# Performance work log

Hardware: AMD Instinct MI355X
Metric: run time of the kernel (lower is better)

The kernel has to match this reference:

```python
import jax, jax.numpy as jnp
import numpy as np
import math

B, M, C = 256, 256, 1024
ALPHA = 0.1

def setup_inputs() -> dict:
    key = jax.random.key(0)
    k1, k2 = jax.random.split(key)
    input_encoded = jax.random.normal(k1, (B, C), dtype=jnp.float32)
    memory_mean = jax.random.normal(k2, (M, C), dtype=jnp.float32)
    return {"input_encoded": input_encoded, "memory_mean": memory_mean}

def reference(input_encoded, memory_mean):
    b, c = input_encoded.shape
    m = memory_mean.shape[0]
    # ---- write_to_memory ----
    # similarity of each input with each prior memory slot: [B, M]
    sims = jnp.einsum('bc,mc->bm', input_encoded, memory_mean)
    closest_idx = jnp.argmax(sims, axis=1)                      # [B]
    sel = memory_mean[closest_idx]                              # [B, C]
    new_row = (1.0 - ALPHA) * sel + ALPHA * input_encoded       # [B, C]
    onehot = (jnp.arange(m)[None, :] == closest_idx[:, None])   # [B, M] bool
    mem = jnp.broadcast_to(memory_mean[None], (b, m, c))
    updated_memory = jnp.where(onehot[:, :, None], new_row[:, None, :], mem)  # [B, M, C]
    dkl_write = 0.5 * jnp.sum((input_encoded - sel) ** 2, axis=1)             # [B]
    # ---- read_with_encoded_input ----
    scale = 1.0 / math.sqrt(c)
    scores = jnp.einsum('bc,bmc->bm', input_encoded, updated_memory) * scale  # [B, M]
    attn = jax.nn.softmax(scores, axis=1)
    z_read = jnp.einsum('bm,bmc->bc', attn, updated_memory)                   # [B, C]
    dkl_read = 0.5 * jnp.sum((z_read - input_encoded) ** 2, axis=1)           # [B]
    kl_div = dkl_write + dkl_read
    return z_read, updated_memory, kl_div
```

## Files before the change

### kernel.cpp

```cpp
#include <hip/hip_runtime.h>
#include <math.h>

#define B_DIM 256
#define M_DIM 256
#define C_DIM 1024
#define C4 256
#define Z_OFF   0
#define UM_OFF  (B_DIM * C_DIM)
#define KL_OFF  (UM_OFF + B_DIM * M_DIM * C_DIM)
#define SCALE   0.03125f

typedef float nfloat4 __attribute__((ext_vector_type(4)));

__device__ __forceinline__ float block_sum8(float v, float* s_w, int lane, int wv) {
    #pragma unroll
    for (int off = 32; off; off >>= 1) v += __shfl_xor(v, off, 64);
    if (lane == 0) s_w[wv] = v;
    __syncthreads();
    float r = s_w[0] + s_w[1] + s_w[2] + s_w[3]
            + s_w[4] + s_w[5] + s_w[6] + s_w[7];
    __syncthreads();
    return r;
}

__device__ __forceinline__ float block_max8(float v, float* s_w, int lane, int wv) {
    #pragma unroll
    for (int off = 32; off; off >>= 1) v = fmaxf(v, __shfl_xor(v, off, 64));
    if (lane == 0) s_w[wv] = v;
    __syncthreads();
    float r = fmaxf(fmaxf(fmaxf(s_w[0], s_w[1]), fmaxf(s_w[2], s_w[3])),
                    fmaxf(fmaxf(s_w[4], s_w[5]), fmaxf(s_w[6], s_w[7])));
    __syncthreads();
    return r;
}

__global__ __launch_bounds__(512) void tm_fused(const float* __restrict__ x,
                                                const float* __restrict__ mem,
                                                float* __restrict__ out) {
    const int b = blockIdx.x;
    const int t = threadIdx.x;
    const int lane = t & 63;
    const int wv = t >> 6;

    __shared__ float4 s_x4[C4];
    __shared__ float  s_sims[M_DIM];
    __shared__ float  s_attn[M_DIM];
    __shared__ float4 s_z4[C4];
    __shared__ float  s_w[8];
    __shared__ float  s_av[4];
    __shared__ int    s_ai[4];
    __shared__ int    s_idx;
    __shared__ float  s_vidx;

    const float4* mem4 = (const float4*)mem;
    const float4* x4row = (const float4*)(x + (size_t)b * C_DIM);

    float4 xt = make_float4(0.f, 0.f, 0.f, 0.f);
    float p = 0.f;
    if (t < C4) {
        xt = x4row[t];
        s_x4[t] = xt;
        p = xt.x * xt.x + xt.y * xt.y + xt.z * xt.z + xt.w * xt.w;
    }
    const float n2 = block_sum8(p, s_w, lane, wv);

    float4 xr0 = s_x4[lane];
    float4 xr1 = s_x4[lane + 64];
    float4 xr2 = s_x4[lane + 128];
    float4 xr3 = s_x4[lane + 192];
    for (int i = 0; i < 32; ++i) {
        const int m = (i << 3) | wv;
        const float4* mr = mem4 + (size_t)m * C4;
        float4 a0 = mr[lane];
        float4 a1 = mr[lane + 64];
        float4 a2 = mr[lane + 128];
        float4 a3 = mr[lane + 192];
        float acc = a0.x * xr0.x + a0.y * xr0.y + a0.z * xr0.z + a0.w * xr0.w
                  + a1.x * xr1.x + a1.y * xr1.y + a1.z * xr1.z + a1.w * xr1.w
                  + a2.x * xr2.x + a2.y * xr2.y + a2.z * xr2.z + a2.w * xr2.w
                  + a3.x * xr3.x + a3.y * xr3.y + a3.z * xr3.z + a3.w * xr3.w;
        #pragma unroll
        for (int off = 32; off; off >>= 1) acc += __shfl_xor(acc, off, 64);
        if (lane == 0) s_sims[m] = acc;
    }
    __syncthreads();

    float av = -INFINITY;
    int   ai = 0x7fffffff;
    if (t < M_DIM) { av = s_sims[t]; ai = t; }
    #pragma unroll
    for (int off = 32; off; off >>= 1) {
        float ov = __shfl_xor(av, off, 64);
        int   oi = __shfl_xor(ai, off, 64);
        if (ov > av || (ov == av && oi < ai)) { av = ov; ai = oi; }
    }
    if (lane == 0 && wv < 4) { s_av[wv] = av; s_ai[wv] = ai; }
    __syncthreads();
    if (t == 0) {
        float bv = s_av[0]; int bi = s_ai[0];
        #pragma unroll
        for (int w = 1; w < 4; ++w) {
            float v2 = s_av[w]; int i2 = s_ai[w];
            if (v2 > bv || (v2 == bv && i2 < bi)) { bv = v2; bi = i2; }
        }
        s_idx = bi; s_vidx = bv;
    }
    __syncthreads();
    const int idx = s_idx;
    const float sim_idx = s_vidx;

    float sc = -INFINITY;
    if (t < M_DIM)
        sc = (t == idx) ? (0.9f * sim_idx + 0.1f * n2) * SCALE
                        : s_sims[t] * SCALE;
    const float mx = block_max8(sc, s_w, lane, wv);
    float e = (t < M_DIM) ? expf(sc - mx) : 0.f;
    const float esum = block_sum8(e, s_w, lane, wv);
    if (t < M_DIM) s_attn[t] = e / esum;

    float dwp = 0.f;
    if (t < C4) {
        float4 sl = mem4[(size_t)idx * C4 + t];
        float d0 = xt.x - sl.x, d1 = xt.y - sl.y, d2 = xt.z - sl.z, d3 = xt.w - sl.w;
        dwp = d0 * d0 + d1 * d1 + d2 * d2 + d3 * d3;
    }
    const float dw = block_sum8(dwp, s_w, lane, wv);

    const int tc = t & 255;
    const int mbase = (t >> 8) << 7;
    const float4 xc = s_x4[tc];
    float4 z = make_float4(0.f, 0.f, 0.f, 0.f);
    nfloat4* um4 = (nfloat4*)((float4*)(out + UM_OFF) + (size_t)b * M_DIM * C4 + tc);
    for (int i = 0; i < 128; ++i) {
        const int m = mbase + i;
        float4 v = mem4[(size_t)m * C4 + tc];
        if (m == idx) {
            v.x = 0.9f * v.x + 0.1f * xc.x;
            v.y = 0.9f * v.y + 0.1f * xc.y;
            v.z = 0.9f * v.z + 0.1f * xc.z;
            v.w = 0.9f * v.w + 0.1f * xc.w;
        }
        const float a = s_attn[m];
        z.x = fmaf(a, v.x, z.x);
        z.y = fmaf(a, v.y, z.y);
        z.z = fmaf(a, v.z, z.z);
        z.w = fmaf(a, v.w, z.w);
        nfloat4 nv = { v.x, v.y, v.z, v.w };
        __builtin_nontemporal_store(nv, um4 + (size_t)m * C4);
    }

    if (t >= 256) s_z4[tc] = z;
    __syncthreads();
    float drp = 0.f;
    if (t < 256) {
        float4 zo = s_z4[tc];
        z.x += zo.x; z.y += zo.y; z.z += zo.z; z.w += zo.w;
        float d0 = z.x - xc.x, d1 = z.y - xc.y, d2 = z.z - xc.z, d3 = z.w - xc.w;
        drp = d0 * d0 + d1 * d1 + d2 * d2 + d3 * d3;
        ((float4*)(out + Z_OFF))[(size_t)b * C4 + t] = z;
    }
    const float dr = block_sum8(drp, s_w, lane, wv);

    if (t == 0) out[KL_OFF + b] = 0.5f * (dw + dr);
}

extern "C" void kernel_launch(void* const* d_in, const int* in_sizes, int n_in,
                              void* d_out, int out_size, void* d_ws, size_t ws_size,
                              hipStream_t stream) {
    const float* x   = (const float*)d_in[0];
    const float* mem = (const float*)d_in[1];
    float* out = (float*)d_out;

    tm_fused<<<dim3(B_DIM), dim3(512), 0, stream>>>(x, mem, out);
}
```

Before: 70.95 us.

## Use 1024-thread blocks, split memory rows four ways, fold selected-row update algebraically

Doubles the threads per block so each block handles its batch row with 16 waves. Each quarter of the threads now covers 64 memory rows instead of 128, and the partial z sums are combined through shared memory. The attention accumulation now uses the original memory row, and the alpha update of the selected row is added once at the end as attn[idx]*0.1*(x - sel). This takes the conditional out of the dependency chain, and the loop is unrolled by 4. The aim is more memory-level parallelism on the large updated-memory write stream, at the cost of wider block-level reductions and more shared memory.

```diff
diff --git a/kernel.cpp b/kernel.cpp
--- a/kernel.cpp
+++ b/kernel.cpp
@@ -12,64 +12,66 @@
 
 typedef float nfloat4 __attribute__((ext_vector_type(4)));
 
-__device__ __forceinline__ float block_sum8(float v, float* s_w, int lane, int wv) {
+__device__ __forceinline__ float block_sum16(float v, float* s_w, int lane, int wv) {
     #pragma unroll
     for (int off = 32; off; off >>= 1) v += __shfl_xor(v, off, 64);
     if (lane == 0) s_w[wv] = v;
     __syncthreads();
-    float r = s_w[0] + s_w[1] + s_w[2] + s_w[3]
-            + s_w[4] + s_w[5] + s_w[6] + s_w[7];
+    float r = 0.f;
+    #pragma unroll
+    for (int w = 0; w < 16; ++w) r += s_w[w];
     __syncthreads();
     return r;
 }
 
-__device__ __forceinline__ float block_max8(float v, float* s_w, int lane, int wv) {
+__device__ __forceinline__ float block_max16(float v, float* s_w, int lane, int wv) {
     #pragma unroll
     for (int off = 32; off; off >>= 1) v = fmaxf(v, __shfl_xor(v, off, 64));
     if (lane == 0) s_w[wv] = v;
     __syncthreads();
-    float r = fmaxf(fmaxf(fmaxf(s_w[0], s_w[1]), fmaxf(s_w[2], s_w[3])),
-                    fmaxf(fmaxf(s_w[4], s_w[5]), fmaxf(s_w[6], s_w[7])));
+    float r = s_w[0];
+    #pragma unroll
+    for (int w = 1; w < 16; ++w) r = fmaxf(r, s_w[w]);
     __syncthreads();
     return r;
 }
 
-__global__ __launch_bounds__(512) void tm_fused(const float* __restrict__ x,
-                                                const float* __restrict__ mem,
-                                                float* __restrict__ out) {
+__global__ __launch_bounds__(1024) void tm_fused(const float* __restrict__ x,
+                                                 const float* __restrict__ mem,
+                                                 float* __restrict__ out) {
     const int b = blockIdx.x;
     const int t = threadIdx.x;
     const int lane = t & 63;
     const int wv = t >> 6;
 
     __shared__ float4 s_x4[C4];
+    __shared__ float4 s_d4[C4];
+    __shared__ float4 s_z4[3][C4];
     __shared__ float  s_sims[M_DIM];
     __shared__ float  s_attn[M_DIM];
-    __shared__ float4 s_z4[C4];
-    __shared__ float  s_w[8];
+    __shared__ float  s_w[16];
     __shared__ float  s_av[4];
     __shared__ int    s_ai[4];
     __shared__ int    s_idx;
     __shared__ float  s_vidx;
 
     const float4* mem4 = (const float4*)mem;
-    const float4* x4row = (const float4*)(x + (size_t)b * C_DIM);
 
     float4 xt = make_float4(0.f, 0.f, 0.f, 0.f);
     float p = 0.f;
     if (t < C4) {
-        xt = x4row[t];
+        xt = ((const float4*)(x + (size_t)b * C_DIM))[t];
         s_x4[t] = xt;
         p = xt.x * xt.x + xt.y * xt.y + xt.z * xt.z + xt.w * xt.w;
     }
-    const float n2 = block_sum8(p, s_w, lane, wv);
+    const float n2 = block_sum16(p, s_w, lane, wv);
 
     float4 xr0 = s_x4[lane];
     float4 xr1 = s_x4[lane + 64];
     float4 xr2 = s_x4[lane + 128];
     float4 xr3 = s_x4[lane + 192];
-    for (int i = 0; i < 32; ++i) {
-        const int m = (i << 3) | wv;
+    for (int i = 0; i < 16; ++i) {
+        const int m = (i << 4) | wv;
         const float4* mr = mem4 + (size_t)m * C4;
         float4 a0 = mr[lane];
         float4 a1 = mr[lane + 64];
@@ -88,13 +90,15 @@
     float av = -INFINITY;
     int   ai = 0x7fffffff;
     if (t < M_DIM) { av = s_sims[t]; ai = t; }
-    #pragma unroll
-    for (int off = 32; off; off >>= 1) {
-        float ov = __shfl_xor(av, off, 64);
-        int   oi = __shfl_xor(ai, off, 64);
-        if (ov > av || (ov == av && oi < ai)) { av = ov; ai = oi; }
+    if (wv < 4) {
+        #pragma unroll
+        for (int off = 32; off; off >>= 1) {
+            float ov = __shfl_xor(av, off, 64);
+            int   oi = __shfl_xor(ai, off, 64);
+            if (ov > av || (ov == av && oi < ai)) { av = ov; ai = oi; }
+        }
+        if (lane == 0) { s_av[wv] = av; s_ai[wv] = ai; }
     }
-    if (lane == 0 && wv < 4) { s_av[wv] = av; s_ai[wv] = ai; }
     __syncthreads();
     if (t == 0) {
         float bv = s_av[0]; int bi = s_ai[0];
@@ -113,53 +117,66 @@
     if (t < M_DIM)
         sc = (t == idx) ? (0.9f * sim_idx + 0.1f * n2) * SCALE
                         : s_sims[t] * SCALE;
-    const float mx = block_max8(sc, s_w, lane, wv);
+    const float mx = block_max16(sc, s_w, lane, wv);
     float e = (t < M_DIM) ? expf(sc - mx) : 0.f;
-    const float esum = block_sum8(e, s_w, lane, wv);
+    const float esum = block_sum16(e, s_w, lane, wv);
     if (t < M_DIM) s_attn[t] = e / esum;
 
     float dwp = 0.f;
     if (t < C4) {
         float4 sl = mem4[(size_t)idx * C4 + t];
-        float d0 = xt.x - sl.x, d1 = xt.y - sl.y, d2 = xt.z - sl.z, d3 = xt.w - sl.w;
-        dwp = d0 * d0 + d1 * d1 + d2 * d2 + d3 * d3;
+        float4 d;
+        d.x = xt.x - sl.x; d.y = xt.y - sl.y; d.z = xt.z - sl.z; d.w = xt.w - sl.w;
+        s_d4[t] = d;
+        dwp = d.x * d.x + d.y * d.y + d.z * d.z + d.w * d.w;
     }
-    const float dw = block_sum8(dwp, s_w, lane, wv);
+    const float dw = block_sum16(dwp, s_w, lane, wv);
 
     const int tc = t & 255;
-    const int mbase = (t >> 8) << 7;
+    const int mq = t >> 8;
+    const int mbase = mq << 6;
     const float4 xc = s_x4[tc];
     float4 z = make_float4(0.f, 0.f, 0.f, 0.f);
     nfloat4* um4 = (nfloat4*)((float4*)(out + UM_OFF) + (size_t)b * M_DIM * C4 + tc);
-    for (int i = 0; i < 128; ++i) {
+    #pragma unroll 4
+    for (int i = 0; i < 64; ++i) {
         const int m = mbase + i;
         float4 v = mem4[(size_t)m * C4 + tc];
+        const float a = s_attn[m];
+        z.x = fmaf(a, v.x, z.x);
+        z.y = fmaf(a, v.y, z.y);
+        z.z = fmaf(a, v.z, z.z);
+        z.w = fmaf(a, v.w, z.w);
         if (m == idx) {
             v.x = 0.9f * v.x + 0.1f * xc.x;
             v.y = 0.9f * v.y + 0.1f * xc.y;
             v.z = 0.9f * v.z + 0.1f * xc.z;
             v.w = 0.9f * v.w + 0.1f * xc.w;
         }
-        const float a = s_attn[m];
-        z.x = fmaf(a, v.x, z.x);
-        z.y = fmaf(a, v.y, z.y);
-        z.z = fmaf(a, v.z, z.z);
-        z.w = fmaf(a, v.w, z.w);
         nfloat4 nv = { v.x, v.y, v.z, v.w };
         __builtin_nontemporal_store(nv, um4 + (size_t)m * C4);
     }
 
-    if (t >= 256) s_z4[tc] = z;
+    if (mq) s_z4[mq - 1][tc] = z;
     __syncthreads();
     float drp = 0.f;
     if (t < 256) {
-        float4 zo = s_z4[tc];
-        z.x += zo.x; z.y += zo.y; z.z += zo.z; z.w += zo.w;
+        float4 z1 = s_z4[0][tc], z2 = s_z4[1][tc], z3 = s_z4[2][tc];
+        z.x += z1.x + z2.x + z3.x;
+        z.y += z1.y + z2.y + z3.y;
+        z.z += z1.z + z2.z + z3.z;
+        z.w += z1.w + z2.w + z3.w;
+        const float aidx = s_attn[idx] * 0.1f;
+        float4 d = s_d4[tc];
+        z.x = fmaf(aidx, d.x, z.x);
+        z.y = fmaf(aidx, d.y, z.y);
+        z.z = fmaf(aidx, d.z, z.z);
+        z.w = fmaf(aidx, d.w, z.w);
         float d0 = z.x - xc.x, d1 = z.y - xc.y, d2 = z.z - xc.z, d3 = z.w - xc.w;
         drp = d0 * d0 + d1 * d1 + d2 * d2 + d3 * d3;
-        ((float4*)(out + Z_OFF))[(size_t)b * C4 + t] = z;
+        ((float4*)(out + Z_OFF))[(size_t)b * C4 + tc] = z;
     }
-    const float dr = block_sum8(drp, s_w, lane, wv);
+    const float dr = block_sum16(drp, s_w, lane, wv);
 
     if (t == 0) out[KL_OFF + b] = 0.5f * (dw + dr);
 }
@@ -171,5 +188,5 @@
     const float* mem = (const float*)d_in[1];
     float* out = (float*)d_out;
 
-    tm_fused<<<dim3(B_DIM), dim3(512), 0, stream>>>(x, mem, out);
+    tm_fused<<<dim3(B_DIM), dim3(1024), 0, stream>>>(x, mem, out);
 }
```

New measurement: 67.83 us. 1.05x faster.

## Split into streaming copy+sims kernel and batched finish kernel

Applied to the files above, without the earlier changes.

Replaces the single per-batch kernel with two kernels. The first uses a 256x8 grid to stream memory rows into the updated-memory output while computing similarities, writing them into the z output region as scratch. The second handles four batch rows per block: it does argmax, overwrites only the selected row with the blended update, and computes softmax and z_read with a rank-one correction, so each memory read is shared across four rows. The aim is more parallelism on the 256MB write-dominated stream and less redundant work in the read phase. The cost is an extra launch and a dependency on the first kernel's scratch output.

```diff
diff --git a/kernel.cpp b/kernel.cpp
--- a/kernel.cpp
+++ b/kernel.cpp
@@ -4,164 +4,282 @@
 #define B_DIM 256
 #define M_DIM 256
 #define C_DIM 1024
-#define C4 256
-#define Z_OFF   0
-#define UM_OFF  (B_DIM * C_DIM)
-#define KL_OFF  (UM_OFF + B_DIM * M_DIM * C_DIM)
-#define SCALE   0.03125f
+#define C4    256
+#define UM_OFF (B_DIM * C_DIM)
+#define KL_OFF (UM_OFF + B_DIM * M_DIM * C_DIM)
+#define SCALE  0.03125f
 
 typedef float nfloat4 __attribute__((ext_vector_type(4)));
 
-__device__ __forceinline__ float block_sum8(float v, float* s_w, int lane, int wv) {
-    #pragma unroll
-    for (int off = 32; off; off >>= 1) v += __shfl_xor(v, off, 64);
-    if (lane == 0) s_w[wv] = v;
-    __syncthreads();
-    float r = s_w[0] + s_w[1] + s_w[2] + s_w[3]
-            + s_w[4] + s_w[5] + s_w[6] + s_w[7];
-    __syncthreads();
-    return r;
-}
-
-__device__ __forceinline__ float block_max8(float v, float* s_w, int lane, int wv) {
-    #pragma unroll
-    for (int off = 32; off; off >>= 1) v = fmaxf(v, __shfl_xor(v, off, 64));
-    if (lane == 0) s_w[wv] = v;
-    __syncthreads();
-    float r = fmaxf(fmaxf(fmaxf(s_w[0], s_w[1]), fmaxf(s_w[2], s_w[3])),
-                    fmaxf(fmaxf(s_w[4], s_w[5]), fmaxf(s_w[6], s_w[7])));
-    __syncthreads();
-    return r;
-}
-
-__global__ __launch_bounds__(512) void tm_fused(const float* __restrict__ x,
-                                                const float* __restrict__ mem,
-                                                float* __restrict__ out) {
+__device__ __forceinline__ void nt_store4(float4 v, nfloat4* p) {
+    nfloat4 n = {v.x, v.y, v.z, v.w};
+    __builtin_nontemporal_store(n, p);
+}
+
+__global__ __launch_bounds__(256) void tm_stream(const float* __restrict__ x,
+                                                 const float* __restrict__ mem,
+                                                 float* __restrict__ out) {
     const int b = blockIdx.x;
+    const int q = blockIdx.y;
     const int t = threadIdx.x;
     const int lane = t & 63;
     const int wv = t >> 6;
 
-    __shared__ float4 s_x4[C4];
-    __shared__ float  s_sims[M_DIM];
-    __shared__ float  s_attn[M_DIM];
-    __shared__ float4 s_z4[C4];
-    __shared__ float  s_w[8];
-    __shared__ float  s_av[4];
-    __shared__ int    s_ai[4];
-    __shared__ int    s_idx;
-    __shared__ float  s_vidx;
+    __shared__ float4 s_x[C4];
+    s_x[t] = ((const float4*)(x + (size_t)b * C_DIM))[t];
+    __syncthreads();
+    const float4 xr0 = s_x[lane];
+    const float4 xr1 = s_x[lane + 64];
+    const float4 xr2 = s_x[lane + 128];
+    const float4 xr3 = s_x[lane + 192];
 
     const float4* mem4 = (const float4*)mem;
-    const float4* x4row = (const float4*)(x + (size_t)b * C_DIM);
-
-    float4 xt = make_float4(0.f, 0.f, 0.f, 0.f);
-    float p = 0.f;
-    if (t < C4) {
-        xt = x4row[t];
-        s_x4[t] = xt;
-        p = xt.x * xt.x + xt.y * xt.y + xt.z * xt.z + xt.w * xt.w;
-    }
-    const float n2 = block_sum8(p, s_w, lane, wv);
-
-    float4 xr0 = s_x4[lane];
-    float4 xr1 = s_x4[lane + 64];
-    float4 xr2 = s_x4[lane + 128];
-    float4 xr3 = s_x4[lane + 192];
-    for (int i = 0; i < 32; ++i) {
-        const int m = (i << 3) | wv;
+    nfloat4* um4 = (nfloat4*)(out + UM_OFF) + (size_t)b * M_DIM * C4;
+    float* simsrow = out + (size_t)b * C_DIM;
+
+    const int m0 = (q << 5) | (wv << 3);
+    #pragma unroll
+    for (int i = 0; i < 8; ++i) {
+        const int m = m0 + i;
         const float4* mr = mem4 + (size_t)m * C4;
         float4 a0 = mr[lane];
         float4 a1 = mr[lane + 64];
         float4 a2 = mr[lane + 128];
         float4 a3 = mr[lane + 192];
-        float acc = a0.x * xr0.x + a0.y * xr0.y + a0.z * xr0.z + a0.w * xr0.w
-                  + a1.x * xr1.x + a1.y * xr1.y + a1.z * xr1.z + a1.w * xr1.w
-                  + a2.x * xr2.x + a2.y * xr2.y + a2.z * xr2.z + a2.w * xr2.w
-                  + a3.x * xr3.x + a3.y * xr3.y + a3.z * xr3.z + a3.w * xr3.w;
+        float p0 = a0.x*xr0.x + a0.y*xr0.y + a0.z*xr0.z + a0.w*xr0.w;
+        float p1 = a1.x*xr1.x + a1.y*xr1.y + a1.z*xr1.z + a1.w*xr1.w;
+        float p2 = a2.x*xr2.x + a2.y*xr2.y + a2.z*xr2.z + a2.w*xr2.w;
+        float p3 = a3.x*xr3.x + a3.y*xr3.y + a3.z*xr3.z + a3.w*xr3.w;
+        float acc = (p0 + p1) + (p2 + p3);
         #pragma unroll
         for (int off = 32; off; off >>= 1) acc += __shfl_xor(acc, off, 64);
-        if (lane == 0) s_sims[m] = acc;
-    }
-    __syncthreads();
-
-    float av = -INFINITY;
-    int   ai = 0x7fffffff;
-    if (t < M_DIM) { av = s_sims[t]; ai = t; }
+        nfloat4* dst = um4 + (size_t)m * C4;
+        nt_store4(a0, dst + lane);
+        nt_store4(a1, dst + lane + 64);
+        nt_store4(a2, dst + lane + 128);
+        nt_store4(a3, dst + lane + 192);
+        if (lane == 0) simsrow[m] = acc;
+    }
+}
+
+__device__ __forceinline__ float4 bsum4(float4 v, float4* s_w, int lane, int wv) {
     #pragma unroll
     for (int off = 32; off; off >>= 1) {
-        float ov = __shfl_xor(av, off, 64);
-        int   oi = __shfl_xor(ai, off, 64);
-        if (ov > av || (ov == av && oi < ai)) { av = ov; ai = oi; }
-    }
-    if (lane == 0 && wv < 4) { s_av[wv] = av; s_ai[wv] = ai; }
-    __syncthreads();
+        v.x += __shfl_xor(v.x, off, 64);
+        v.y += __shfl_xor(v.y, off, 64);
+        v.z += __shfl_xor(v.z, off, 64);
+        v.w += __shfl_xor(v.w, off, 64);
+    }
+    if (lane == 0) s_w[wv] = v;
+    __syncthreads();
+    float4 r = s_w[0];
+    #pragma unroll
+    for (int w = 1; w < 8; ++w) {
+        r.x += s_w[w].x; r.y += s_w[w].y; r.z += s_w[w].z; r.w += s_w[w].w;
+    }
+    __syncthreads();
+    return r;
+}
+
+__device__ __forceinline__ float4 bmax4(float4 v, float4* s_w, int lane, int wv) {
+    #pragma unroll
+    for (int off = 32; off; off >>= 1) {
+        v.x = fmaxf(v.x, __shfl_xor(v.x, off, 64));
+        v.y = fmaxf(v.y, __shfl_xor(v.y, off, 64));
+        v.z = fmaxf(v.z, __shfl_xor(v.z, off, 64));
+        v.w = fmaxf(v.w, __shfl_xor(v.w, off, 64));
+    }
+    if (lane == 0) s_w[wv] = v;
+    __syncthreads();
+    float4 r = s_w[0];
+    #pragma unroll
+    for (int w = 1; w < 8; ++w) {
+        r.x = fmaxf(r.x, s_w[w].x); r.y = fmaxf(r.y, s_w[w].y);
+        r.z = fmaxf(r.z, s_w[w].z); r.w = fmaxf(r.w, s_w[w].w);
+    }
+    __syncthreads();
+    return r;
+}
+
+__global__ __launch_bounds__(512) void tm_finish(const float* __restrict__ x,
+                                                 const float* __restrict__ mem,
+                                                 float* __restrict__ out) {
+    const int g = blockIdx.x;
+    const int t = threadIdx.x;
+    const int lane = t & 63;
+    const int wv = t >> 6;
+    const int tc = t & 255;
+    const int h  = t >> 8;
+
+    __shared__ float4 s_x[4][C4];
+    __shared__ float  s_sims[4][M_DIM];
+    __shared__ float4 s_d[4][C4];
+    __shared__ float  s_attn[4][M_DIM];
+    __shared__ float4 s_zp[4][C4];
+    __shared__ float4 s_w4[8];
+    __shared__ float  s_av[8];
+    __shared__ int    s_ai[8];
+    __shared__ int    s_idx[4];
+
+    const float4* mem4 = (const float4*)mem;
+
+    #pragma unroll
+    for (int j = 0; j < 4; ++j) {
+        const int b = (g << 2) + j;
+        if (h == 0) s_x[j][tc] = ((const float4*)(x + (size_t)b * C_DIM))[tc];
+        else        s_sims[j][tc] = out[(size_t)b * C_DIM + tc];
+    }
+    __syncthreads();
+
+    float4 pv = make_float4(0.f, 0.f, 0.f, 0.f);
+    if (h == 0) {
+        float4 x0 = s_x[0][tc], x1 = s_x[1][tc], x2 = s_x[2][tc], x3 = s_x[3][tc];
+        pv.x = x0.x*x0.x + x0.y*x0.y + x0.z*x0.z + x0.w*x0.w;
+        pv.y = x1.x*x1.x + x1.y*x1.y + x1.z*x1.z + x1.w*x1.w;
+        pv.z = x2.x*x2.x + x2.y*x2.y + x2.z*x2.z + x2.w*x2.w;
+        pv.w = x3.x*x3.x + x3.y*x3.y + x3.z*x3.z + x3.w*x3.w;
+    }
+    float4 n2v = bsum4(pv, s_w4, lane, wv);
+    const float n2_[4] = {n2v.x, n2v.y, n2v.z, n2v.w};
+
+    #pragma unroll
+    for (int j = 0; j < 4; ++j) {
+        float av = -INFINITY; int ai = 0x7fffffff;
+        if (h == 0) { av = s_sims[j][tc]; ai = tc; }
+        #pragma unroll
+        for (int off = 32; off; off >>= 1) {
+            float ov = __shfl_xor(av, off, 64);
+            int   oi = __shfl_xor(ai, off, 64);
+            if (ov > av || (ov == av && oi < ai)) { av = ov; ai = oi; }
+        }
+        if (lane == 0) { s_av[wv] = av; s_ai[wv] = ai; }
+        __syncthreads();
+        if (t == 0) {
+            float bv = s_av[0]; int bi = s_ai[0];
+            #pragma unroll
+            for (int w = 1; w < 8; ++w) {
+                float v2 = s_av[w]; int i2 = s_ai[w];
+                if (v2 > bv || (v2 == bv && i2 < bi)) { bv = v2; bi = i2; }
+            }
+            s_idx[j] = bi;
+        }
+        __syncthreads();
+    }
+
+    float4 dwp = make_float4(0.f, 0.f, 0.f, 0.f);
+    #pragma unroll
+    for (int j = 0; j < 4; ++j) {
+        const int b = (g << 2) + j;
+        const int idx = s_idx[j];
+        if (h == 0) {
+            float4 sl = mem4[(size_t)idx * C4 + tc];
+            float4 xv = s_x[j][tc];
+            float4 d = make_float4(xv.x - sl.x, xv.y - sl.y, xv.z - sl.z, xv.w - sl.w);
+            s_d[j][tc] = d;
+            float dd = d.x*d.x + d.y*d.y + d.z*d.z + d.w*d.w;
+            if      (j == 0) dwp.x = dd;
+            else if (j == 1) dwp.y = dd;
+            else if (j == 2) dwp.z = dd;
+            else             dwp.w = dd;
+            float4 bl = make_float4(0.9f*sl.x + 0.1f*xv.x, 0.9f*sl.y + 0.1f*xv.y,
+                                    0.9f*sl.z + 0.1f*xv.z, 0.9f*sl.w + 0.1f*xv.w);
+            nt_store4(bl, (nfloat4*)(out + UM_OFF) + ((size_t)b * M_DIM + idx) * C4 + tc);
+        }
+    }
+    float4 dwv = bsum4(dwp, s_w4, lane, wv);
+    const float dw_[4] = {dwv.x, dwv.y, dwv.z, dwv.w};
+
+    float4 scv = make_float4(-INFINITY, -INFINITY, -INFINITY, -INFINITY);
+    if (h == 0) {
+        #pragma unroll
+        for (int j = 0; j < 4; ++j) {
+            const int idx = s_idx[j];
+            float sc = (tc == idx) ? (0.9f * s_sims[j][idx] + 0.1f * n2_[j]) * SCALE
+                                   : s_sims[j][tc] * SCALE;
+            if      (j == 0) scv.x = sc;
+            else if (j == 1) scv.y = sc;
+            else if (j == 2) scv.z = sc;
+            else             scv.w = sc;
+        }
+    }
+    float4 mxv = bmax4(scv, s_w4, lane, wv);
+    float4 ev = make_float4(0.f, 0.f, 0.f, 0.f);
+    if (h == 0) {
+        ev.x = expf(scv.x - mxv.x);
+        ev.y = expf(scv.y - mxv.y);
+        ev.z = expf(scv.z - mxv.z);
+        ev.w = expf(scv.w - mxv.w);
+    }
+    float4 esv = bsum4(ev, s_w4, lane, wv);
+    if (h == 0) {
+        s_attn[0][tc] = ev.x / esv.x;
+        s_attn[1][tc] = ev.y / esv.y;
+        s_attn[2][tc] = ev.z / esv.z;
+        s_attn[3][tc] = ev.w / esv.w;
+    }
+    __syncthreads();
+
+    float4 z0 = make_float4(0.f,0.f,0.f,0.f), z1 = z0, z2 = z0, z3 = z0;
+    #pragma unroll 4
+    for (int i = 0; i < 128; ++i) {
+        const int m = (h << 7) + i;
+        float4 v = mem4[(size_t)m * C4 + tc];
+        const float a0 = s_attn[0][m], a1 = s_attn[1][m];
+        const float a2 = s_attn[2][m], a3 = s_attn[3][m];
+        z0.x = fmaf(a0, v.x, z0.x); z0.y = fmaf(a0, v.y, z0.y);
+        z0.z = fmaf(a0, v.z, z0.z); z0.w = fmaf(a0, v.w, z0.w);
+        z1.x = fmaf(a1, v.x, z1.x); z1.y = fmaf(a1, v.y, z1.y);
+        z1.z = fmaf(a1, v.z, z1.z); z1.w = fmaf(a1, v.w, z1.w);
+        z2.x = fmaf(a2, v.x, z2.x); z2.y = fmaf(a2, v.y, z2.y);
+        z2.z = fmaf(a2, v.z, z2.z); z2.w = fmaf(a2, v.w, z2.w);
+        z3.x = fmaf(a3, v.x, z3.x); z3.y = fmaf(a3, v.y, z3.y);
+        z3.z = fmaf(a3, v.z, z3.z); z3.w = fmaf(a3, v.w, z3.w);
+    }
+    if (h == 1) { s_zp[0][tc] = z0; s_zp[1][tc] = z1; s_zp[2][tc] = z2; s_zp[3][tc] = z3; }
+    __syncthreads();
+
+    float4 drp = make_float4(0.f, 0.f, 0.f, 0.f);
+    if (h == 0) {
+        float4 o0 = s_zp[0][tc], o1 = s_zp[1][tc], o2 = s_zp[2][tc], o3 = s_zp[3][tc];
+        z0.x += o0.x; z0.y += o0.y; z0.z += o0.z; z0.w += o0.w;
+        z1.x += o1.x; z1.y += o1.y; z1.z += o1.z; z1.w += o1.w;
+        z2.x += o2.x; z2.y += o2.y; z2.z += o2.z; z2.w += o2.w;
+        z3.x += o3.x; z3.y += o3.y; z3.z += o3.z; z3.w += o3.w;
+        const float ax0 = s_attn[0][s_idx[0]] * 0.1f;
+        const float ax1 = s_attn[1][s_idx[1]] * 0.1f;
+        const float ax2 = s_attn[2][s_idx[2]] * 0.1f;
+        const float ax3 = s_attn[3][s_idx[3]] * 0.1f;
+        float4 d0 = s_d[0][tc], d1 = s_d[1][tc], d2 = s_d[2][tc], d3 = s_d[3][tc];
+        z0.x = fmaf(ax0, d0.x, z0.x); z0.y = fmaf(ax0, d0.y, z0.y);
+        z0.z = fmaf(ax0, d0.z, z0.z); z0.w = fmaf(ax0, d0.w, z0.w);
+        z1.x = fmaf(ax1, d1.x, z1.x); z1.y = fmaf(ax1, d1.y, z1.y);
+        z1.z = fmaf(ax1, d1.z, z1.z); z1.w = fmaf(ax1, d1.w, z1.w);
+        z2.x = fmaf(ax2, d2.x, z2.x); z2.y = fmaf(ax2, d2.y, z2.y);
+        z2.z = fmaf(ax2, d2.z, z2.z); z2.w = fmaf(ax2, d2.w, z2.w);
+        z3.x = fmaf(ax3, d3.x, z3.x); z3.y = fmaf(ax3, d3.y, z3.y);
+        z3.z = fmaf(ax3, d3.z, z3.z); z3.w = fmaf(ax3, d3.w, z3.w);
+        float4 x0 = s_x[0][tc], x1 = s_x[1][tc], x2 = s_x[2][tc], x3 = s_x[3][tc];
+        float e0x = z0.x-x0.x, e0y = z0.y-x0.y, e0z = z0.z-x0.z, e0w = z0.w-x0.w;
+        float e1x = z1.x-x1.x, e1y = z1.y-x1.y, e1z = z1.z-x1.z, e1w = z1.w-x1.w;
+        float e2x = z2.x-x2.x, e2y = z2.y-x2.y, e2z = z2.z-x2.z, e2w = z2.w-x2.w;
+        float e3x = z3.x-x3.x, e3y = z3.y-x3.y, e3z = z3.z-x3.z, e3w = z3.w-x3.w;
+        drp.x = e0x*e0x + e0y*e0y + e0z*e0z + e0w*e0w;
+        drp.y = e1x*e1x + e1y*e1y + e1z*e1z + e1w*e1w;
+        drp.z = e2x*e2x + e2y*e2y + e2z*e2z + e2w*e2w;
+        drp.w = e3x*e3x + e3y*e3y + e3z*e3z + e3w*e3w;
+        float4* zout = (float4*)out;
+        zout[((size_t)((g << 2) + 0)) * C4 + tc] = z0;
+        zout[((size_t)((g << 2) + 1)) * C4 + tc] = z1;
+        zout[((size_t)((g << 2) + 2)) * C4 + tc] = z2;
+        zout[((size_t)((g << 2) + 3)) * C4 + tc] = z3;
+    }
+    float4 drv = bsum4(drp, s_w4, lane, wv);
     if (t == 0) {
-        float bv = s_av[0]; int bi = s_ai[0];
-        #pragma unroll
-        for (int w = 1; w < 4; ++w) {
-            float v2 = s_av[w]; int i2 = s_ai[w];
-            if (v2 > bv || (v2 == bv && i2 < bi)) { bv = v2; bi = i2; }
-        }
-        s_idx = bi; s_vidx = bv;
-    }
-    __syncthreads();
-    const int idx = s_idx;
-    const float sim_idx = s_vidx;
-
-    float sc = -INFINITY;
-    if (t < M_DIM)
-        sc = (t == idx) ? (0.9f * sim_idx + 0.1f * n2) * SCALE
-                        : s_sims[t] * SCALE;
-    const float mx = block_max8(sc, s_w, lane, wv);
-    float e = (t < M_DIM) ? expf(sc - mx) : 0.f;
-    const float esum = block_sum8(e, s_w, lane, wv);
-    if (t < M_DIM) s_attn[t] = e / esum;
-
-    float dwp = 0.f;
-    if (t < C4) {
-        float4 sl = mem4[(size_t)idx * C4 + t];
-        float d0 = xt.x - sl.x, d1 = xt.y - sl.y, d2 = xt.z - sl.z, d3 = xt.w - sl.w;
-        dwp = d0 * d0 + d1 * d1 + d2 * d2 + d3 * d3;
-    }
-    const float dw = block_sum8(dwp, s_w, lane, wv);
-
-    const int tc = t & 255;
-    const int mbase = (t >> 8) << 7;
-    const float4 xc = s_x4[tc];
-    float4 z = make_float4(0.f, 0.f, 0.f, 0.f);
-    nfloat4* um4 = (nfloat4*)((float4*)(out + UM_OFF) + (size_t)b * M_DIM * C4 + tc);
-    for (int i = 0; i < 128; ++i) {
-        const int m = mbase + i;
-        float4 v = mem4[(size_t)m * C4 + tc];
-        if (m == idx) {
-            v.x = 0.9f * v.x + 0.1f * xc.x;
-            v.y = 0.9f * v.y + 0.1f * xc.y;
-            v.z = 0.9f * v.z + 0.1f * xc.z;
-            v.w = 0.9f * v.w + 0.1f * xc.w;
-        }
-        const float a = s_attn[m];
-        z.x = fmaf(a, v.x, z.x);
-        z.y = fmaf(a, v.y, z.y);
-        z.z = fmaf(a, v.z, z.z);
-        z.w = fmaf(a, v.w, z.w);
-        nfloat4 nv = { v.x, v.y, v.z, v.w };
-        __builtin_nontemporal_store(nv, um4 + (size_t)m * C4);
-    }
-
-    if (t >= 256) s_z4[tc] = z;
-    __syncthreads();
-    float drp = 0.f;
-    if (t < 256) {
-        float4 zo = s_z4[tc];
-        z.x += zo.x; z.y += zo.y; z.z += zo.z; z.w += zo.w;
-        float d0 = z.x - xc.x, d1 = z.y - xc.y, d2 = z.z - xc.z, d3 = z.w - xc.w;
-        drp = d0 * d0 + d1 * d1 + d2 * d2 + d3 * d3;
-        ((float4*)(out + Z_OFF))[(size_t)b * C4 + t] = z;
-    }
-    const float dr = block_sum8(drp, s_w, lane, wv);
-
-    if (t == 0) out[KL_OFF + b] = 0.5f * (dw + dr);
+        out[KL_OFF + (g << 2) + 0] = 0.5f * (dw_[0] + drv.x);
+        out[KL_OFF + (g << 2) + 1] = 0.5f * (dw_[1] + drv.y);
+        out[KL_OFF + (g << 2) + 2] = 0.5f * (dw_[2] + drv.z);
+        out[KL_OFF + (g << 2) + 3] = 0.5f * (dw_[3] + drv.w);
+    }
 }
 
 extern "C" void kernel_launch(void* const* d_in, const int* in_sizes, int n_in,
@@ -171,5 +289,6 @@
     const float* mem = (const float*)d_in[1];
     float* out = (float*)d_out;
 
-    tm_fused<<<dim3(B_DIM), dim3(512), 0, stream>>>(x, mem, out);
-}
+    tm_stream<<<dim3(B_DIM, 8), dim3(256), 0, stream>>>(x, mem, out);
+    tm_finish<<<dim3(64), dim3(512), 0, stream>>>(x, mem, out);
+}
```

After: 69.54 us. 1.02x faster.

## Stagger memory copy before sims on odd blocks to overlap compute with stores

Applied to the files above, without the earlier changes.

Odd-indexed blocks copy the full memory bank into their updated_memory slice before the similarity/argmax phase, then later overwrite only the selected row. Even blocks keep the original fused copy-and-accumulate loop. The intent is to desynchronize write-heavy and compute/latency-bound phases across blocks so the write bandwidth is busy during reductions. The z accumulation now uses the original memory rows and adds a rank-one correction (0.1*attn[idx]*(x-sel)). The risk is that the odd blocks reread mem, adding L2 read traffic, and that their duplicate row write is ordered after the bulk store.

```diff
diff --git a/kernel.cpp b/kernel.cpp
--- a/kernel.cpp
+++ b/kernel.cpp
@@ -4,163 +4,223 @@
 #define B_DIM 256
 #define M_DIM 256
 #define C_DIM 1024
-#define C4 256
-#define Z_OFF   0
-#define UM_OFF  (B_DIM * C_DIM)
-#define KL_OFF  (UM_OFF + B_DIM * M_DIM * C_DIM)
-#define SCALE   0.03125f
+#define C4    256
+#define UM_OFF (B_DIM * C_DIM)
+#define KL_OFF (UM_OFF + B_DIM * M_DIM * C_DIM)
+#define SCALE  0.03125f
 
 typedef float nfloat4 __attribute__((ext_vector_type(4)));
 
-__device__ __forceinline__ float block_sum8(float v, float* s_w, int lane, int wv) {
-    #pragma unroll
-    for (int off = 32; off; off >>= 1) v += __shfl_xor(v, off, 64);
-    if (lane == 0) s_w[wv] = v;
-    __syncthreads();
-    float r = s_w[0] + s_w[1] + s_w[2] + s_w[3]
-            + s_w[4] + s_w[5] + s_w[6] + s_w[7];
-    __syncthreads();
-    return r;
-}
-
-__device__ __forceinline__ float block_max8(float v, float* s_w, int lane, int wv) {
-    #pragma unroll
-    for (int off = 32; off; off >>= 1) v = fmaxf(v, __shfl_xor(v, off, 64));
-    if (lane == 0) s_w[wv] = v;
-    __syncthreads();
-    float r = fmaxf(fmaxf(fmaxf(s_w[0], s_w[1]), fmaxf(s_w[2], s_w[3])),
-                    fmaxf(fmaxf(s_w[4], s_w[5]), fmaxf(s_w[6], s_w[7])));
-    __syncthreads();
-    return r;
-}
-
-__global__ __launch_bounds__(512) void tm_fused(const float* __restrict__ x,
-                                                const float* __restrict__ mem,
-                                                float* __restrict__ out) {
+__device__ __forceinline__ void nt_store4(float4 v, float4* p) {
+    nfloat4 n = {v.x, v.y, v.z, v.w};
+    __builtin_nontemporal_store(n, (nfloat4*)p);
+}
+__device__ __forceinline__ float dot4(float4 a, float4 b) {
+    return a.x*b.x + a.y*b.y + a.z*b.z + a.w*b.w;
+}
+
+__global__ __launch_bounds__(512) void tm_stag(const float* __restrict__ x,
+                                               const float* __restrict__ mem,
+                                               float* __restrict__ out) {
     const int b = blockIdx.x;
     const int t = threadIdx.x;
     const int lane = t & 63;
     const int wv = t >> 6;
-
-    __shared__ float4 s_x4[C4];
+    const int tc = t & 255;
+    const int h  = t >> 8;
+    const bool late = (b & 1);
+
+    __shared__ float4 s_x[C4];
+    __shared__ float4 s_zp[C4];
     __shared__ float  s_sims[M_DIM];
     __shared__ float  s_attn[M_DIM];
-    __shared__ float4 s_z4[C4];
     __shared__ float  s_w[8];
-    __shared__ float  s_av[4];
-    __shared__ int    s_ai[4];
-    __shared__ int    s_idx;
-    __shared__ float  s_vidx;
+    __shared__ float  s_av[8];
+    __shared__ int    s_ai[8];
+    __shared__ int    s_idxs;
 
     const float4* mem4 = (const float4*)mem;
-    const float4* x4row = (const float4*)(x + (size_t)b * C_DIM);
-
-    float4 xt = make_float4(0.f, 0.f, 0.f, 0.f);
-    float p = 0.f;
-    if (t < C4) {
-        xt = x4row[t];
-        s_x4[t] = xt;
-        p = xt.x * xt.x + xt.y * xt.y + xt.z * xt.z + xt.w * xt.w;
-    }
-    const float n2 = block_sum8(p, s_w, lane, wv);
-
-    float4 xr0 = s_x4[lane];
-    float4 xr1 = s_x4[lane + 64];
-    float4 xr2 = s_x4[lane + 128];
-    float4 xr3 = s_x4[lane + 192];
-    for (int i = 0; i < 32; ++i) {
-        const int m = (i << 3) | wv;
-        const float4* mr = mem4 + (size_t)m * C4;
-        float4 a0 = mr[lane];
-        float4 a1 = mr[lane + 64];
-        float4 a2 = mr[lane + 128];
-        float4 a3 = mr[lane + 192];
-        float acc = a0.x * xr0.x + a0.y * xr0.y + a0.z * xr0.z + a0.w * xr0.w
-                  + a1.x * xr1.x + a1.y * xr1.y + a1.z * xr1.z + a1.w * xr1.w
-                  + a2.x * xr2.x + a2.y * xr2.y + a2.z * xr2.z + a2.w * xr2.w
-                  + a3.x * xr3.x + a3.y * xr3.y + a3.z * xr3.z + a3.w * xr3.w;
-        #pragma unroll
-        for (int off = 32; off; off >>= 1) acc += __shfl_xor(acc, off, 64);
-        if (lane == 0) s_sims[m] = acc;
+    float4* umrow = (float4*)(out + UM_OFF) + (size_t)b * (M_DIM * C4);
+
+    if (late) {
+        #pragma unroll 4
+        for (int i = 0; i < 128; ++i) {
+            const int m = (h << 7) + i;
+            float4 v = mem4[(m << 8) + tc];
+            nt_store4(v, umrow + (m << 8) + tc);
+        }
+    }
+
+    float4 xv = make_float4(0.f, 0.f, 0.f, 0.f);
+    if (h == 0) {
+        xv = ((const float4*)(x + (size_t)b * C_DIM))[tc];
+        s_x[tc] = xv;
     }
     __syncthreads();
 
-    float av = -INFINITY;
-    int   ai = 0x7fffffff;
-    if (t < M_DIM) { av = s_sims[t]; ai = t; }
-    #pragma unroll
-    for (int off = 32; off; off >>= 1) {
-        float ov = __shfl_xor(av, off, 64);
-        int   oi = __shfl_xor(ai, off, 64);
-        if (ov > av || (ov == av && oi < ai)) { av = ov; ai = oi; }
-    }
-    if (lane == 0 && wv < 4) { s_av[wv] = av; s_ai[wv] = ai; }
+    float n2;
+    {
+        float p = (h == 0) ? dot4(xv, xv) : 0.f;
+        #pragma unroll
+        for (int off = 32; off; off >>= 1) p += __shfl_xor(p, off, 64);
+        if (lane == 0) s_w[wv] = p;
+        __syncthreads();
+        n2 = s_w[0]+s_w[1]+s_w[2]+s_w[3]+s_w[4]+s_w[5]+s_w[6]+s_w[7];
+        __syncthreads();
+    }
+
+    {
+        const float4 xr0 = s_x[lane];
+        const float4 xr1 = s_x[lane + 64];
+        const float4 xr2 = s_x[lane + 128];
+        const float4 xr3 = s_x[lane + 192];
+        #pragma unroll 4
+        for (int i = 0; i < 32; ++i) {
+            const int m = (wv << 5) | i;
+            const float4* mr = mem4 + (m << 8);
+            float acc = dot4(mr[lane],     xr0) + dot4(mr[lane+64],  xr1)
+                      + dot4(mr[lane+128], xr2) + dot4(mr[lane+192], xr3);
+            #pragma unroll
+            for (int off = 32; off; off >>= 1) acc += __shfl_xor(acc, off, 64);
+            if (lane == 0) s_sims[m] = acc;
+        }
+    }
     __syncthreads();
-    if (t == 0) {
-        float bv = s_av[0]; int bi = s_ai[0];
-        #pragma unroll
-        for (int w = 1; w < 4; ++w) {
-            float v2 = s_av[w]; int i2 = s_ai[w];
-            if (v2 > bv || (v2 == bv && i2 < bi)) { bv = v2; bi = i2; }
-        }
-        s_idx = bi; s_vidx = bv;
-    }
-    __syncthreads();
-    const int idx = s_idx;
-    const float sim_idx = s_vidx;
+
+    {
+        float av = -INFINITY; int ai = 0x7fffffff;
+        if (h == 0) { av = s_sims[tc]; ai = tc; }
+        #pragma unroll
+        for (int off = 32; off; off >>= 1) {
+            float ov = __shfl_xor(av, off, 64);
+            int   oi = __shfl_xor(ai, off, 64);
+            if (ov > av || (ov == av && oi < ai)) { av = ov; ai = oi; }
+        }
+        if (lane == 0) { s_av[wv] = av; s_ai[wv] = ai; }
+        __syncthreads();
+        if (t == 0) {
+            float bv = s_av[0]; int bi = s_ai[0];
+            #pragma unroll
+            for (int w = 1; w < 4; ++w) {
+                float v2 = s_av[w]; int i2 = s_ai[w];
+                if (v2 > bv || (v2 == bv && i2 < bi)) { bv = v2; bi = i2; }
+            }
+            s_idxs = bi;
+        }
+        __syncthreads();
+    }
+    const int idx = s_idxs;
 
     float sc = -INFINITY;
-    if (t < M_DIM)
-        sc = (t == idx) ? (0.9f * sim_idx + 0.1f * n2) * SCALE
-                        : s_sims[t] * SCALE;
-    const float mx = block_max8(sc, s_w, lane, wv);
-    float e = (t < M_DIM) ? expf(sc - mx) : 0.f;
-    const float esum = block_sum8(e, s_w, lane, wv);
-    if (t < M_DIM) s_attn[t] = e / esum;
-
-    float dwp = 0.f;
-    if (t < C4) {
-        float4 sl = mem4[(size_t)idx * C4 + t];
-        float d0 = xt.x - sl.x, d1 = xt.y - sl.y, d2 = xt.z - sl.z, d3 = xt.w - sl.w;
-        dwp = d0 * d0 + d1 * d1 + d2 * d2 + d3 * d3;
-    }
-    const float dw = block_sum8(dwp, s_w, lane, wv);
-
-    const int tc = t & 255;
-    const int mbase = (t >> 8) << 7;
-    const float4 xc = s_x4[tc];
+    if (h == 0)
+        sc = (tc == idx) ? (0.9f * s_sims[idx] + 0.1f * n2) * SCALE
+                         : s_sims[tc] * SCALE;
+    float mx;
+    {
+        float v = sc;
+        #pragma unroll
+        for (int off = 32; off; off >>= 1) v = fmaxf(v, __shfl_xor(v, off, 64));
+        if (lane == 0) s_w[wv] = v;
+        __syncthreads();
+        mx = fmaxf(fmaxf(fmaxf(s_w[0], s_w[1]), fmaxf(s_w[2], s_w[3])),
+                   fmaxf(fmaxf(s_w[4], s_w[5]), fmaxf(s_w[6], s_w[7])));
+        __syncthreads();
+    }
+    float e = (h == 0) ? expf(sc - mx) : 0.f;
+    float esum;
+    {
+        float v = e;
+        #pragma unroll
+        for (int off = 32; off; off >>= 1) v += __shfl_xor(v, off, 64);
+        if (lane == 0) s_w[wv] = v;
+        __syncthreads();
+        esum = s_w[0]+s_w[1]+s_w[2]+s_w[3]+s_w[4]+s_w[5]+s_w[6]+s_w[7];
+        __syncthreads();
+    }
+    if (h == 0) s_attn[tc] = e / esum;
+
+    float4 d = make_float4(0.f, 0.f, 0.f, 0.f);
+    float dw;
+    {
+        float dd = 0.f;
+        if (h == 0) {
+            float4 sl = mem4[(idx << 8) + tc];
+            d = make_float4(xv.x - sl.x, xv.y - sl.y, xv.z - sl.z, xv.w - sl.w);
+            dd = dot4(d, d);
+        }
+        float v = dd;
+        #pragma unroll
+        for (int off = 32; off; off >>= 1) v += __shfl_xor(v, off, 64);
+        if (lane == 0) s_w[wv] = v;
+        __syncthreads();
+        dw = s_w[0]+s_w[1]+s_w[2]+s_w[3]+s_w[4]+s_w[5]+s_w[6]+s_w[7];
+        __syncthreads();
+    }
+
     float4 z = make_float4(0.f, 0.f, 0.f, 0.f);
-    nfloat4* um4 = (nfloat4*)((float4*)(out + UM_OFF) + (size_t)b * M_DIM * C4 + tc);
-    for (int i = 0; i < 128; ++i) {
-        const int m = mbase + i;
-        float4 v = mem4[(size_t)m * C4 + tc];
-        if (m == idx) {
-            v.x = 0.9f * v.x + 0.1f * xc.x;
-            v.y = 0.9f * v.y + 0.1f * xc.y;
-            v.z = 0.9f * v.z + 0.1f * xc.z;
-            v.w = 0.9f * v.w + 0.1f * xc.w;
-        }
-        const float a = s_attn[m];
-        z.x = fmaf(a, v.x, z.x);
-        z.y = fmaf(a, v.y, z.y);
-        z.z = fmaf(a, v.z, z.z);
-        z.w = fmaf(a, v.w, z.w);
-        nfloat4 nv = { v.x, v.y, v.z, v.w };
-        __builtin_nontemporal_store(nv, um4 + (size_t)m * C4);
-    }
-
-    if (t >= 256) s_z4[tc] = z;
+    if (!late) {
+        #pragma unroll 4
+        for (int i = 0; i < 128; ++i) {
+            const int m = (h << 7) + i;
+            float4 v = mem4[(m << 8) + tc];
+            const float a = s_attn[m];
+            z.x = fmaf(a, v.x, z.x);
+            z.y = fmaf(a, v.y, z.y);
+            z.z = fmaf(a, v.z, z.z);
+            z.w = fmaf(a, v.w, z.w);
+            if (m == idx) {
+                float4 xb = s_x[tc];
+                v.x = 0.9f*v.x + 0.1f*xb.x;
+                v.y = 0.9f*v.y + 0.1f*xb.y;
+                v.z = 0.9f*v.z + 0.1f*xb.z;
+                v.w = 0.9f*v.w + 0.1f*xb.w;
+            }
+            nt_store4(v, umrow + (m << 8) + tc);
+        }
+    } else {
+        #pragma unroll 4
+        for (int i = 0; i < 128; ++i) {
+            const int m = (h << 7) + i;
+            float4 v = mem4[(m << 8) + tc];
+            const float a = s_attn[m];
+            z.x = fmaf(a, v.x, z.x);
+            z.y = fmaf(a, v.y, z.y);
+            z.z = fmaf(a, v.z, z.z);
+            z.w = fmaf(a, v.w, z.w);
+        }
+        if (h == (idx >> 7)) {
+            float4 sl = mem4[(idx << 8) + tc];
+            float4 xb = s_x[tc];
+            float4 bl = make_float4(0.9f*sl.x + 0.1f*xb.x, 0.9f*sl.y + 0.1f*xb.y,
+                                    0.9f*sl.z + 0.1f*xb.z, 0.9f*sl.w + 0.1f*xb.w);
+            nt_store4(bl, umrow + (idx << 8) + tc);
+        }
+    }
+
+    if (h == 1) s_zp[tc] = z;
     __syncthreads();
     float drp = 0.f;
-    if (t < 256) {
-        float4 zo = s_z4[tc];
+    if (h == 0) {
+        float4 zo = s_zp[tc];
         z.x += zo.x; z.y += zo.y; z.z += zo.z; z.w += zo.w;
-        float d0 = z.x - xc.x, d1 = z.y - xc.y, d2 = z.z - xc.z, d3 = z.w - xc.w;
-        drp = d0 * d0 + d1 * d1 + d2 * d2 + d3 * d3;
-        ((float4*)(out + Z_OFF))[(size_t)b * C4 + t] = z;
-    }
-    const float dr = block_sum8(drp, s_w, lane, wv);
-
+        const float aidx = s_attn[idx] * 0.1f;
+        z.x = fmaf(aidx, d.x, z.x);
+        z.y = fmaf(aidx, d.y, z.y);
+        z.z = fmaf(aidx, d.z, z.z);
+        z.w = fmaf(aidx, d.w, z.w);
+        float e0 = z.x - xv.x, e1 = z.y - xv.y, e2 = z.z - xv.z, e3 = z.w - xv.w;
+        drp = e0*e0 + e1*e1 + e2*e2 + e3*e3;
+        ((float4*)out)[(size_t)b * C4 + tc] = z;
+    }
+    float dr;
+    {
+        float v = drp;
+        #pragma unroll
+        for (int off = 32; off; off >>= 1) v += __shfl_xor(v, off, 64);
+        if (lane == 0) s_w[wv] = v;
+        __syncthreads();
+        dr = s_w[0]+s_w[1]+s_w[2]+s_w[3]+s_w[4]+s_w[5]+s_w[6]+s_w[7];
+    }
     if (t == 0) out[KL_OFF + b] = 0.5f * (dw + dr);
 }
 
@@ -171,5 +231,5 @@
     const float* mem = (const float*)d_in[1];
     float* out = (float*)d_out;
 
-    tm_fused<<<dim3(B_DIM), dim3(512), 0, stream>>>(x, mem, out);
-}
+    tm_stag<<<dim3(B_DIM), dim3(512), 0, stream>>>(x, mem, out);
+}
```

New measurement: 69.72 us. About the same (-1.7%).
